# Kernel tuning notes

Measured on AMD Instinct MI355X. Metric: run time of the kernel, lower is better.

The kernel has to match this reference:

```python
import jax, jax.numpy as jnp
import numpy as np

B, V_IN, V_OUT, C_IN, C_OUT, K, NNZ = 16, 1024, 4096, 128, 256, 18, 16384

def setup_inputs() -> dict:
    key = jax.random.key(0)
    ks = jax.random.split(key, 10)
    def lin(k, fan_in, fan_out):
        s = 1.0 / np.sqrt(fan_in)
        return jax.random.normal(k, (fan_in, fan_out), jnp.float32) * s
    return {
        "x": jax.random.normal(ks[0], (B, V_IN, C_IN), jnp.float32),
        "vals": jax.random.uniform(ks[1], (NNZ,), jnp.float32),
        "W1": lin(ks[2], 1 * C_IN, C_OUT),
        "b1": jnp.zeros((C_OUT,), jnp.float32),
        "Wd3": lin(ks[3], (K // 3) * C_IN, C_OUT // 4),
        "bd3": jnp.zeros((C_OUT // 4,), jnp.float32),
        "W2d3": lin(ks[4], (K // 3 * 2) * C_IN, C_OUT // 4),
        "b2d3": jnp.zeros((C_OUT // 4,), jnp.float32),
        "Wf": lin(ks[5], K * C_IN, C_OUT // 2),
        "bf": jnp.zeros((C_OUT // 2,), jnp.float32),
        "rows": jax.random.randint(ks[6], (NNZ,), 0, V_OUT, jnp.int32),
        "cols": jax.random.randint(ks[7], (NNZ,), 0, V_IN, jnp.int32),
        "spiral_idx": jax.random.randint(ks[8], (V_OUT, K), 0, V_OUT, jnp.int32),
    }

def _pool(x, rows, cols, vals, dim_size):
    # sparse upsample: gather cols, scale, scatter-add to rows
    gathered = x[:, cols, :] * vals[None, :, None]  # [B, nnz, C]
    return jnp.zeros((x.shape[0], dim_size, x.shape[2]), x.dtype).at[:, rows, :].add(gathered)

def _spiral_conv(feat, idx, W, b):
    # gather fixed spiral neighborhoods then shared linear layer
    Bz, V, C = feat.shape[0], idx.shape[0], feat.shape[2]
    g = feat[:, idx.reshape(-1), :].reshape(Bz, V, idx.shape[1] * C)  # [B, V, K*C]
    return g @ W + b

def reference(x, vals, W1, b1, Wd3, bd3, W2d3, b2d3, Wf, bf, rows, cols, spiral_idx):
    out = _pool(x, rows, cols, vals, V_OUT)  # [B, V_OUT, C_IN]
    k = spiral_idx.shape[1]
    short_cut = _spiral_conv(out, spiral_idx[:, :1], W1, b1)
    p_d3 = _spiral_conv(out, spiral_idx[:, : k // 3], Wd3, bd3)
    p_2d3 = _spiral_conv(out, spiral_idx[:, : k // 3 * 2], W2d3, b2d3)
    p = _spiral_conv(out, spiral_idx, Wf, bf)
    f = jnp.concatenate((p, p_2d3, p_d3), axis=2)  # [B, V_OUT, C_OUT]
    return jax.nn.relu(short_cut + f)
```

## Files before the change

### kernel.cpp

```cpp
#include <hip/hip_runtime.h>
#include <hip/hip_bf16.h>

#define B_SZ   16
#define V_IN   1024
#define V_OUT  4096
#define C_IN   128
#define C_OUT  256
#define K_NB   18
#define NNZ    16384
#define K_GEMM (K_NB * C_IN)
#define BK     64
#define NKT    (K_GEMM / BK)

typedef __attribute__((ext_vector_type(8))) short bf16x8;
typedef __attribute__((ext_vector_type(4))) float f32x4;

#define GLOAD16(src, dst) __builtin_amdgcn_global_load_lds( \
    (const __attribute__((address_space(1))) unsigned int*)(src), \
    (__attribute__((address_space(3))) unsigned int*)(dst), 16, 0, 0)

#define MFMA16(a_, b_, c_) __builtin_amdgcn_mfma_f32_16x16x32_bf16((a_), (b_), (c_), 0, 0, 0)

__global__ __launch_bounds__(256) void hist_wcomb_kernel(
    const int* __restrict__ rows, int* __restrict__ counts,
    const float* __restrict__ W1, const float* __restrict__ Wd3,
    const float* __restrict__ W2d3, const float* __restrict__ Wf,
    const float* __restrict__ b1, const float* __restrict__ bd3,
    const float* __restrict__ b2d3, const float* __restrict__ bf,
    __hip_bfloat16* __restrict__ wTs, float* __restrict__ bias) {
    const int t = threadIdx.x;
    if (blockIdx.x < 64) {
        int n = blockIdx.x * 256 + t;
        atomicAdd(&counts[rows[n]], 1);
        return;
    }
    const int blk = blockIdx.x - 64;
    if (blk == NKT * 4) {
        float v = b1[t];
        if (t < 128)      v += bf[t];
        else if (t < 192) v += b2d3[t - 128];
        else              v += bd3[t - 192];
        bias[t] = v;
        return;
    }
    const int kt = blk >> 2, part = blk & 3;
    __shared__ __hip_bfloat16 img[4096];
    const int k0 = kt * 64;

    auto put = [&](int cl, int col7, int kl, float v) {
        int kb    = (kl >> 3) << 4;
        int kslot = kb ^ (col7 << 4);
        int idx   = (((cl << 3) | (kslot >> 4)) << 3) | (kl & 7);
        img[idx] = __float2bfloat16(v);
    };

    if (part < 2) {
        const int cbase = part << 6;
        for (int i = t; i < 4096; i += 256) {
            int kl = i >> 6, cl = i & 63;
            int col = cbase + cl, r = k0 + kl;
            float v = Wf[r * 128 + col];
            if (r < 128) v += W1[r * 256 + col];
            put(cl, col & 7, kl, v);
        }
    } else if (part == 2) {
        for (int i = t; i < 4096; i += 256) {
            int kl = i >> 6, cl = i & 63;
            int r = k0 + kl;
            float v = (r < 1536) ? W2d3[r * 64 + cl] : 0.f;
            if (r < 128) v += W1[r * 256 + 128 + cl];
            put(cl, cl & 7, kl, v);
        }
    } else {
        for (int i = t; i < 4096; i += 256) {
            int kl = i >> 6, cl = i & 63;
            int r = k0 + kl;
            float v = (r < 768) ? Wd3[r * 64 + cl] : 0.f;
            if (r < 128) v += W1[r * 256 + 192 + cl];
            put(cl, cl & 7, kl, v);
        }
    }
    __syncthreads();
    ulonglong2* dst = (ulonglong2*)(wTs + (size_t)kt * 16384 + part * 4096);
    const ulonglong2* srcv = (const ulonglong2*)img;
#pragma unroll
    for (int i = t; i < 512; i += 256) dst[i] = srcv[i];
}

__global__ void scan_kernel(const int* __restrict__ counts, int* offsets, int* cursor) {
    __shared__ int wsum[16];
    int t = threadIdx.x;
    int lane = t & 63, wid = t >> 6;
    int base4 = t * 4;
    int c0 = counts[base4], c1 = counts[base4 + 1], c2 = counts[base4 + 2], c3 = counts[base4 + 3];
    int tot = c0 + c1 + c2 + c3;
    int v = tot;
#pragma unroll
    for (int d = 1; d < 64; d <<= 1) {
        int u = __shfl_up(v, d);
        if (lane >= d) v += u;
    }
    if (lane == 63) wsum[wid] = v;
    __syncthreads();
    int wbase = 0;
#pragma unroll
    for (int w = 0; w < 16; ++w) wbase += (w < wid) ? wsum[w] : 0;
    int incl = wbase + v;
    int excl = incl - tot;
    offsets[base4]     = excl;
    offsets[base4 + 1] = excl + c0;
    offsets[base4 + 2] = excl + c0 + c1;
    offsets[base4 + 3] = excl + c0 + c1 + c2;
    cursor[base4]     = excl;
    cursor[base4 + 1] = excl + c0;
    cursor[base4 + 2] = excl + c0 + c1;
    cursor[base4 + 3] = excl + c0 + c1 + c2;
    if (t == 1023) offsets[V_OUT] = incl;
}

__global__ void fill_kernel(const int* __restrict__ rows, const int* __restrict__ cols,
                            const float* __restrict__ vals, int* cursor,
                            float2* __restrict__ pcv) {
    int n = blockIdx.x * blockDim.x + threadIdx.x;
    if (n < NNZ) {
        int r = rows[n];
        int pos = atomicAdd(&cursor[r], 1);
        pcv[pos] = make_float2(__int_as_float(cols[n]), vals[n]);
    }
}

__global__ __launch_bounds__(512) void pool_kernel(
    const float* __restrict__ x, const int* __restrict__ offsets,
    const float2* __restrict__ pcv, __hip_bfloat16* __restrict__ pool) {
    int r = blockIdx.x;
    int t = threadIdx.x;
    int b = t >> 5, c4 = t & 31;
    int j0 = offsets[r], j1 = offsets[r + 1];
    const float4* xb = (const float4*)x + (size_t)b * (V_IN * 32);
    float4 acc = {0.f, 0.f, 0.f, 0.f};
    for (int j = j0; j < j1; ++j) {
        float2 cv = pcv[j];
        int col = __float_as_int(cv.x);
        float v = cv.y;
        float4 xv = xb[col * 32 + c4];
        acc.x += v * xv.x; acc.y += v * xv.y; acc.z += v * xv.z; acc.w += v * xv.w;
    }
    ushort4 o;
    o.x = __builtin_bit_cast(unsigned short, __float2bfloat16(acc.x));
    o.y = __builtin_bit_cast(unsigned short, __float2bfloat16(acc.y));
    o.z = __builtin_bit_cast(unsigned short, __float2bfloat16(acc.z));
    o.w = __builtin_bit_cast(unsigned short, __float2bfloat16(acc.w));
    ((ushort4*)pool)[((size_t)b * V_OUT + r) * 32 + c4] = o;
}

__global__ __launch_bounds__(1024, 4) void gemm_kernel(
    const __hip_bfloat16* __restrict__ pool,
    const __hip_bfloat16* __restrict__ wTs,
    const float* __restrict__ bias,
    const int* __restrict__ spiral,
    float* __restrict__ out)
{
    __shared__ __align__(16) char smem[149504];
    int* spl = (int*)(smem + 131072);

    const int tid  = threadIdx.x;
    const int lane = tid & 63;
    const int wid  = tid >> 6;
    const int wc   = wid & 3;
    const int wm   = (wid >> 2) << 6;

    const int bid = blockIdx.x;
    const int bm  = ((bid & 7) << 5) + (bid >> 3);
    const int b   = bm >> 4;
    const int v0  = (bm & 15) << 8;

    for (int i = tid; i < 256 * K_NB; i += 1024) spl[i] = spiral[v0 * K_NB + i];
    asm volatile("s_waitcnt vmcnt(0) lgkmcnt(0)" ::: "memory");
    __builtin_amdgcn_s_barrier();

    const char* poolBytes = (const char*)(pool + (size_t)b * V_OUT * C_IN);
    const char* wTsBytes  = (const char*)wTs;
    const int sb = ((tid & 7) << 4) ^ (((tid >> 3) & 7) << 4);

    auto stageA = [&](int kt) {
        const int j   = kt >> 1;
        const int c0b = (kt & 1) << 7;
        char* dst = smem + ((kt & 1) << 15);
#pragma unroll
        for (int ch = 0; ch < 2; ++ch) {
            int flat = (ch << 10) + tid;
            int sidx = spl[(flat >> 3) * K_NB + j];
            GLOAD16(poolBytes + ((size_t)sidx << 8) + (c0b + sb), dst + flat * 16);
        }
    };
    auto stageB = [&](int kt) {
        const char* src = wTsBytes + ((size_t)kt << 15);
        char* dst = smem + 65536 + ((kt & 1) << 15);
#pragma unroll
        for (int ch = 0; ch < 2; ++ch) {
            int off = ((ch << 10) + tid) << 4;
            GLOAD16(src + off, dst + off);
        }
    };

    const int l15   = lane & 15;
    const int swm   = (lane & 7) << 4;
    const int klane = (lane >> 4) << 4;
    const int aBase = (wm + l15) << 7;
    const int bOff0 = (((2 * wc)     << 4) + l15) << 7;
    const int bOff1 = (((2 * wc + 1) << 4) + l15) << 7;
    const int bOff2 = (((8 + wc)     << 4) + l15) << 7;
    const int bOff3 = (((12 + wc)    << 4) + l15) << 7;

    f32x4 acc[4][4] = {};

    stageA(0);
    stageB(0);

    for (int kt = 0; kt < NKT; ++kt) {
        const int s = kt & 1;
        const char* As = smem + (s << 15);
        const char* Bs = smem + 65536 + (s << 15);

        if (kt + 1 < NKT) {
            stageA(kt + 1);
            asm volatile("s_waitcnt vmcnt(2)" ::: "memory");
        } else {
            asm volatile("s_waitcnt vmcnt(0)" ::: "memory");
        }
        __builtin_amdgcn_s_barrier();
        __builtin_amdgcn_sched_barrier(0);

        const bool doMid   = kt < 24;
        const bool doShort = kt < 12;

#pragma unroll
        for (int ks = 0; ks < 2; ++ks) {
            const int kk = (ks * 64 + klane) ^ swm;
            bf16x8 a0 = *(const bf16x8*)(As + aBase + (0 << 11) + kk);
            bf16x8 a1 = *(const bf16x8*)(As + aBase + (1 << 11) + kk);
            bf16x8 a2 = *(const bf16x8*)(As + aBase + (2 << 11) + kk);
            bf16x8 a3 = *(const bf16x8*)(As + aBase + (3 << 11) + kk);
            bf16x8 bb0 = *(const bf16x8*)(Bs + bOff0 + kk);
            bf16x8 bb1 = *(const bf16x8*)(Bs + bOff1 + kk);
            __builtin_amdgcn_s_setprio(1);
            acc[0][0] = MFMA16(a0, bb0, acc[0][0]);
            acc[1][0] = MFMA16(a1, bb0, acc[1][0]);
            acc[2][0] = MFMA16(a2, bb0, acc[2][0]);
            acc[3][0] = MFMA16(a3, bb0, acc[3][0]);
            acc[0][1] = MFMA16(a0, bb1, acc[0][1]);
            acc[1][1] = MFMA16(a1, bb1, acc[1][1]);
            acc[2][1] = MFMA16(a2, bb1, acc[2][1]);
            acc[3][1] = MFMA16(a3, bb1, acc[3][1]);
            __builtin_amdgcn_s_setprio(0);
            if (doMid) {
                bf16x8 bb2 = *(const bf16x8*)(Bs + bOff2 + kk);
                __builtin_amdgcn_s_setprio(1);
                acc[0][2] = MFMA16(a0, bb2, acc[0][2]);
                acc[1][2] = MFMA16(a1, bb2, acc[1][2]);
                acc[2][2] = MFMA16(a2, bb2, acc[2][2]);
                acc[3][2] = MFMA16(a3, bb2, acc[3][2]);
                __builtin_amdgcn_s_setprio(0);
            }
            if (doShort) {
                bf16x8 bb3 = *(const bf16x8*)(Bs + bOff3 + kk);
                __builtin_amdgcn_s_setprio(1);
                acc[0][3] = MFMA16(a0, bb3, acc[0][3]);
                acc[1][3] = MFMA16(a1, bb3, acc[1][3]);
                acc[2][3] = MFMA16(a2, bb3, acc[2][3]);
                acc[3][3] = MFMA16(a3, bb3, acc[3][3]);
                __builtin_amdgcn_s_setprio(0);
            }
            if (ks == 0 && kt + 1 < NKT) stageB(kt + 1);
        }

        __builtin_amdgcn_s_barrier();
        __builtin_amdgcn_sched_barrier(0);
    }

    const int nt[4] = {2 * wc, 2 * wc + 1, 8 + wc, 12 + wc};
#pragma unroll
    for (int ni = 0; ni < 4; ++ni) {
        int col = (nt[ni] << 4) + l15;
        float bz = bias[col];
#pragma unroll
        for (int mi = 0; mi < 4; ++mi) {
            int row0 = v0 + wm + mi * 16 + ((lane >> 4) << 2);
#pragma unroll
            for (int r4 = 0; r4 < 4; ++r4) {
                float v = acc[mi][ni][r4] + bz;
                out[((size_t)(b * V_OUT + row0 + r4)) * C_OUT + col] = v > 0.f ? v : 0.f;
            }
        }
    }
}

extern "C" void kernel_launch(void* const* d_in, const int* in_sizes, int n_in,
                              void* d_out, int out_size, void* d_ws, size_t ws_size,
                              hipStream_t stream) {
    const float* x     = (const float*)d_in[0];
    const float* vals  = (const float*)d_in[1];
    const float* W1    = (const float*)d_in[2];
    const float* b1    = (const float*)d_in[3];
    const float* Wd3   = (const float*)d_in[4];
    const float* bd3   = (const float*)d_in[5];
    const float* W2d3  = (const float*)d_in[6];
    const float* b2d3  = (const float*)d_in[7];
    const float* Wf    = (const float*)d_in[8];
    const float* bf    = (const float*)d_in[9];
    const int*   rows  = (const int*)d_in[10];
    const int*   cols  = (const int*)d_in[11];
    const int*   spiral= (const int*)d_in[12];
    float* out = (float*)d_out;

    char* ws = (char*)d_ws;
    __hip_bfloat16* pool = (__hip_bfloat16*)ws;
    __hip_bfloat16* wTs  = (__hip_bfloat16*)(ws + 16777216);
    float* bias          = (float*)(ws + 16777216 + 1179648);
    int*   counts        = (int*)(ws + 16777216 + 1179648 + 1024);
    int*   offsets       = counts + V_OUT;
    int*   cursor        = offsets + V_OUT + 4;
    float2* pcv          = (float2*)(cursor + V_OUT);

    hipMemsetAsync(counts, 0, V_OUT * sizeof(int), stream);
    hist_wcomb_kernel<<<64 + NKT * 4 + 1, 256, 0, stream>>>(
        rows, counts, W1, Wd3, W2d3, Wf, b1, bd3, b2d3, bf, wTs, bias);
    scan_kernel<<<1, 1024, 0, stream>>>(counts, offsets, cursor);
    fill_kernel<<<NNZ / 256, 256, 0, stream>>>(rows, cols, vals, cursor, pcv);
    pool_kernel<<<V_OUT, 512, 0, stream>>>(x, offsets, pcv, pool);
    gemm_kernel<<<256, 1024, 0, stream>>>(pool, wTs, bias, spiral, out);
}
```

Measured before the change: 103.4 us.

## Load weight fragments directly from global in MFMA layout, triple-buffer A tiles

```diff
diff --git a/kernel.cpp b/kernel.cpp
--- a/kernel.cpp
+++ b/kernel.cpp
@@ -47,10 +47,11 @@
     __shared__ __hip_bfloat16 img[4096];
     const int k0 = kt * 64;
 
-    auto put = [&](int cl, int col7, int kl, float v) {
-        int kb    = (kl >> 3) << 4;
-        int kslot = kb ^ (col7 << 4);
-        int idx   = (((cl << 3) | (kslot >> 4)) << 3) | (kl & 7);
+    auto put = [&](int cl, int kl, float v) {
+        int ks   = kl >> 5;
+        int lane = (cl & 15) | (((kl >> 3) & 3) << 4);
+        int e    = kl & 7;
+        int idx  = ((cl >> 4) << 10) | (ks << 9) | (lane << 3) | e;
         img[idx] = __float2bfloat16(v);
     };
 
@@ -61,7 +62,7 @@
             int col = cbase + cl, r = k0 + kl;
             float v = Wf[r * 128 + col];
             if (r < 128) v += W1[r * 256 + col];
-            put(cl, col & 7, kl, v);
+            put(cl, kl, v);
         }
     } else if (part == 2) {
         for (int i = t; i < 4096; i += 256) {
@@ -69,7 +70,7 @@
             int r = k0 + kl;
             float v = (r < 1536) ? W2d3[r * 64 + cl] : 0.f;
             if (r < 128) v += W1[r * 256 + 128 + cl];
-            put(cl, cl & 7, kl, v);
+            put(cl, kl, v);
         }
     } else {
         for (int i = t; i < 4096; i += 256) {
@@ -77,7 +78,7 @@
             int r = k0 + kl;
             float v = (r < 768) ? Wd3[r * 64 + cl] : 0.f;
             if (r < 128) v += W1[r * 256 + 192 + cl];
-            put(cl, cl & 7, kl, v);
+            put(cl, kl, v);
         }
     }
     __syncthreads();
@@ -160,8 +161,8 @@
     const int* __restrict__ spiral,
     float* __restrict__ out)
 {
-    __shared__ __align__(16) char smem[149504];
-    int* spl = (int*)(smem + 131072);
+    __shared__ __align__(16) char smem[116736];
+    int* spl = (int*)(smem + 98304);
 
     const int tid  = threadIdx.x;
     const int lane = tid & 63;
@@ -182,10 +183,10 @@
     const char* wTsBytes  = (const char*)wTs;
     const int sb = ((tid & 7) << 4) ^ (((tid >> 3) & 7) << 4);
 
-    auto stageA = [&](int kt) {
+    auto stageA = [&](int kt, int slot) {
         const int j   = kt >> 1;
         const int c0b = (kt & 1) << 7;
-        char* dst = smem + ((kt & 1) << 15);
+        char* dst = smem + slot * 32768;
 #pragma unroll
         for (int ch = 0; ch < 2; ++ch) {
             int flat = (ch << 10) + tid;
@@ -193,89 +194,116 @@
             GLOAD16(poolBytes + ((size_t)sidx << 8) + (c0b + sb), dst + flat * 16);
         }
     };
-    auto stageB = [&](int kt) {
-        const char* src = wTsBytes + ((size_t)kt << 15);
-        char* dst = smem + 65536 + ((kt & 1) << 15);
-#pragma unroll
-        for (int ch = 0; ch < 2; ++ch) {
-            int off = ((ch << 10) + tid) << 4;
-            GLOAD16(src + off, dst + off);
-        }
-    };
 
     const int l15   = lane & 15;
     const int swm   = (lane & 7) << 4;
     const int klane = (lane >> 4) << 4;
+    const int kk0   = klane ^ swm;
+    const int kk1   = (64 + klane) ^ swm;
     const int aBase = (wm + l15) << 7;
-    const int bOff0 = (((2 * wc)     << 4) + l15) << 7;
-    const int bOff1 = (((2 * wc + 1) << 4) + l15) << 7;
-    const int bOff2 = (((8 + wc)     << 4) + l15) << 7;
-    const int bOff3 = (((12 + wc)    << 4) + l15) << 7;
+    const int fOff  = lane << 4;
+    const int nt0B  = (2 * wc)     * 2048;
+    const int nt1B  = (2 * wc + 1) * 2048;
+    const int nt2B  = (8 + wc)     * 2048;
+    const int nt3B  = (12 + wc)    * 2048;
 
     f32x4 acc[4][4] = {};
 
-    stageA(0);
-    stageB(0);
-
+    stageA(0, 0);
+
+    int sl = 0;
     for (int kt = 0; kt < NKT; ++kt) {
-        const int s = kt & 1;
-        const char* As = smem + (s << 15);
-        const char* Bs = smem + 65536 + (s << 15);
-
+        const char* As  = smem + sl * 32768;
+        const char* wKt = wTsBytes + ((size_t)kt << 15);
+        const bool doMid = kt < 24, doShort = kt < 12;
+
+        bf16x8 b00, b01, b02, b03, b10, b11, b12, b13;
+        b00 = *(const bf16x8*)(wKt + nt0B + fOff);
+        b01 = *(const bf16x8*)(wKt + nt1B + fOff);
+        b10 = *(const bf16x8*)(wKt + nt0B + 1024 + fOff);
+        b11 = *(const bf16x8*)(wKt + nt1B + 1024 + fOff);
+        if (doMid)   { b02 = *(const bf16x8*)(wKt + nt2B + fOff);
+                       b12 = *(const bf16x8*)(wKt + nt2B + 1024 + fOff); }
+        if (doShort) { b03 = *(const bf16x8*)(wKt + nt3B + fOff);
+                       b13 = *(const bf16x8*)(wKt + nt3B + 1024 + fOff); }
+
+        int nsl = sl + 1; if (nsl == 3) nsl = 0;
         if (kt + 1 < NKT) {
-            stageA(kt + 1);
-            asm volatile("s_waitcnt vmcnt(2)" ::: "memory");
+            stageA(kt + 1, nsl);
+            if (doShort)      asm volatile("s_waitcnt vmcnt(10)" ::: "memory");
+            else if (doMid)   asm volatile("s_waitcnt vmcnt(8)"  ::: "memory");
+            else              asm volatile("s_waitcnt vmcnt(6)"  ::: "memory");
         } else {
-            asm volatile("s_waitcnt vmcnt(0)" ::: "memory");
+            asm volatile("s_waitcnt vmcnt(4)" ::: "memory");
         }
         __builtin_amdgcn_s_barrier();
         __builtin_amdgcn_sched_barrier(0);
 
-        const bool doMid   = kt < 24;
-        const bool doShort = kt < 12;
-
-#pragma unroll
-        for (int ks = 0; ks < 2; ++ks) {
-            const int kk = (ks * 64 + klane) ^ swm;
-            bf16x8 a0 = *(const bf16x8*)(As + aBase + (0 << 11) + kk);
-            bf16x8 a1 = *(const bf16x8*)(As + aBase + (1 << 11) + kk);
-            bf16x8 a2 = *(const bf16x8*)(As + aBase + (2 << 11) + kk);
-            bf16x8 a3 = *(const bf16x8*)(As + aBase + (3 << 11) + kk);
-            bf16x8 bb0 = *(const bf16x8*)(Bs + bOff0 + kk);
-            bf16x8 bb1 = *(const bf16x8*)(Bs + bOff1 + kk);
+        {
+            bf16x8 a0 = *(const bf16x8*)(As + aBase + (0 << 11) + kk0);
+            bf16x8 a1 = *(const bf16x8*)(As + aBase + (1 << 11) + kk0);
+            bf16x8 a2 = *(const bf16x8*)(As + aBase + (2 << 11) + kk0);
+            bf16x8 a3 = *(const bf16x8*)(As + aBase + (3 << 11) + kk0);
             __builtin_amdgcn_s_setprio(1);
-            acc[0][0] = MFMA16(a0, bb0, acc[0][0]);
-            acc[1][0] = MFMA16(a1, bb0, acc[1][0]);
-            acc[2][0] = MFMA16(a2, bb0, acc[2][0]);
-            acc[3][0] = MFMA16(a3, bb0, acc[3][0]);
-            acc[0][1] = MFMA16(a0, bb1, acc[0][1]);
-            acc[1][1] = MFMA16(a1, bb1, acc[1][1]);
-            acc[2][1] = MFMA16(a2, bb1, acc[2][1]);
-            acc[3][1] = MFMA16(a3, bb1, acc[3][1]);
+            acc[0][0] = MFMA16(a0, b00, acc[0][0]);
+            acc[1][0] = MFMA16(a1, b00, acc[1][0]);
+            acc[2][0] = MFMA16(a2, b00, acc[2][0]);
+            acc[3][0] = MFMA16(a3, b00, acc[3][0]);
+            acc[0][1] = MFMA16(a0, b01, acc[0][1]);
+            acc[1][1] = MFMA16(a1, b01, acc[1][1]);
+            acc[2][1] = MFMA16(a2, b01, acc[2][1]);
+            acc[3][1] = MFMA16(a3, b01, acc[3][1]);
             __builtin_amdgcn_s_setprio(0);
             if (doMid) {
-                bf16x8 bb2 = *(const bf16x8*)(Bs + bOff2 + kk);
                 __builtin_amdgcn_s_setprio(1);
-                acc[0][2] = MFMA16(a0, bb2, acc[0][2]);
-                acc[1][2] = MFMA16(a1, bb2, acc[1][2]);
-                acc[2][2] = MFMA16(a2, bb2, acc[2][2]);
-                acc[3][2] = MFMA16(a3, bb2, acc[3][2]);
+                acc[0][2] = MFMA16(a0, b02, acc[0][2]);
+                acc[1][2] = MFMA16(a1, b02, acc[1][2]);
+                acc[2][2] = MFMA16(a2, b02, acc[2][2]);
+                acc[3][2] = MFMA16(a3, b02, acc[3][2]);
                 __builtin_amdgcn_s_setprio(0);
             }
             if (doShort) {
-                bf16x8 bb3 = *(const bf16x8*)(Bs + bOff3 + kk);
                 __builtin_amdgcn_s_setprio(1);
-                acc[0][3] = MFMA16(a0, bb3, acc[0][3]);
-                acc[1][3] = MFMA16(a1, bb3, acc[1][3]);
-                acc[2][3] = MFMA16(a2, bb3, acc[2][3]);
-                acc[3][3] = MFMA16(a3, bb3, acc[3][3]);
+                acc[0][3] = MFMA16(a0, b03, acc[0][3]);
+                acc[1][3] = MFMA16(a1, b03, acc[1][3]);
+                acc[2][3] = MFMA16(a2, b03, acc[2][3]);
+                acc[3][3] = MFMA16(a3, b03, acc[3][3]);
                 __builtin_amdgcn_s_setprio(0);
             }
-            if (ks == 0 && kt + 1 < NKT) stageB(kt + 1);
-        }
-
-        __builtin_amdgcn_s_barrier();
-        __builtin_amdgcn_sched_barrier(0);
+        }
+        {
+            bf16x8 a0 = *(const bf16x8*)(As + aBase + (0 << 11) + kk1);
+            bf16x8 a1 = *(const bf16x8*)(As + aBase + (1 << 11) + kk1);
+            bf16x8 a2 = *(const bf16x8*)(As + aBase + (2 << 11) + kk1);
+            bf16x8 a3 = *(const bf16x8*)(As + aBase + (3 << 11) + kk1);
+            __builtin_amdgcn_s_setprio(1);
+            acc[0][0] = MFMA16(a0, b10, acc[0][0]);
+            acc[1][0] = MFMA16(a1, b10, acc[1][0]);
+            acc[2][0] = MFMA16(a2, b10, acc[2][0]);
+            acc[3][0] = MFMA16(a3, b10, acc[3][0]);
+            acc[0][1] = MFMA16(a0, b11, acc[0][1]);
+            acc[1][1] = MFMA16(a1, b11, acc[1][1]);
+            acc[2][1] = MFMA16(a2, b11, acc[2][1]);
+            acc[3][1] = MFMA16(a3, b11, acc[3][1]);
+            __builtin_amdgcn_s_setprio(0);
+            if (doMid) {
+                __builtin_amdgcn_s_setprio(1);
+                acc[0][2] = MFMA16(a0, b12, acc[0][2]);
+                acc[1][2] = MFMA16(a1, b12, acc[1][2]);
+                acc[2][2] = MFMA16(a2, b12, acc[2][2]);
+                acc[3][2] = MFMA16(a3, b12, acc[3][2]);
+                __builtin_amdgcn_s_setprio(0);
+            }
+            if (doShort) {
+                __builtin_amdgcn_s_setprio(1);
+                acc[0][3] = MFMA16(a0, b13, acc[0][3]);
+                acc[1][3] = MFMA16(a1, b13, acc[1][3]);
+                acc[2][3] = MFMA16(a2, b13, acc[2][3]);
+                acc[3][3] = MFMA16(a3, b13, acc[3][3]);
+                __builtin_amdgcn_s_setprio(0);
+            }
+        }
+        sl = nsl;
     }
 
     const int nt[4] = {2 * wc, 2 * wc + 1, 8 + wc, 12 + wc};
```

New measurement: 107.8 us. +4.3%, slower.
